# Optimization experiments

Measured on AMD Instinct MI355X. Metric: run time of the kernel, lower is better.

## Reference

```python
import jax, jax.numpy as jnp
import numpy as np

N = 100000
E = 1600000
D = 128
EPS = 1e-5


def setup_inputs() -> dict:
    key = jax.random.key(0)
    ks = jax.random.split(key, 6)
    X = jax.random.normal(ks[0], (N, D), dtype=jnp.float32)
    edge_weight = jax.random.uniform(ks[1], (E,), dtype=jnp.float32)
    W = jax.random.normal(ks[2], (2 * D, D), dtype=jnp.float32) * (1.0 / np.sqrt(2 * D))
    b = jax.random.normal(ks[3], (D,), dtype=jnp.float32) * 0.01
    gamma = jnp.ones((D,), dtype=jnp.float32)
    beta = jnp.zeros((D,), dtype=jnp.float32)
    edge_src = jax.random.randint(ks[4], (E,), 0, N, dtype=jnp.int32)
    edge_dst = jax.random.randint(ks[5], (E,), 0, N, dtype=jnp.int32)
    return {"X": X, "edge_weight": edge_weight, "W": W, "b": b,
            "gamma": gamma, "beta": beta,
            "edge_src": edge_src, "edge_dst": edge_dst}


def reference(X, edge_weight, W, b, gamma, beta, edge_src, edge_dst):
    # Pre-LayerNorm over feature dim
    mu = jnp.mean(X, axis=-1, keepdims=True)
    var = jnp.mean(jnp.square(X - mu), axis=-1, keepdims=True)
    H = (X - mu) * jax.lax.rsqrt(var + EPS) * gamma + beta
    # dropout is identity in eval mode
    # sparse neighbor aggregation: neigh[i] = sum_{e: dst[e]=i} w[e] * H[src[e]]
    msgs = edge_weight[:, None] * H[edge_src]          # [E, D]
    neigh = jax.ops.segment_sum(msgs, edge_dst, num_segments=X.shape[0])  # [N, D]
    cat = jnp.concatenate([H, neigh], axis=1)          # [N, 2D]
    out = cat @ W + b                                  # [N, D]
    out = jax.nn.relu(out)
    return out + X                                     # residual (in_dim == out_dim)
```

## Files before the change

### kernel.cpp

```cpp
#include <hip/hip_runtime.h>
#include <hip/hip_bf16.h>

#define N_NODES 100000
#define D 128
#define E_EDGES 1600000

#define BSHIFT 6
#define BROWS 64
#define NBUCK 1563
#define CAP 1536
#define NBLK_S 256
#define SBLK 1024
#define EPB (E_EDGES / NBLK_S)
#define LN_BLOCKS ((N_NODES + 15) / 16)

typedef __attribute__((ext_vector_type(8))) short bf16x8;
typedef __attribute__((ext_vector_type(8))) unsigned short ushort8;
typedef __attribute__((ext_vector_type(4))) float f32x4;

__device__ __forceinline__ float bf2f(unsigned short u) {
    unsigned int x = ((unsigned int)u) << 16;
    return __builtin_bit_cast(float, x);
}
__device__ __forceinline__ unsigned short f2bf(float f) {
    unsigned int x = __builtin_bit_cast(unsigned int, f);
    unsigned int lsb = (x >> 16) & 1u;
    x += 0x7fffu + lsb;
    return (unsigned short)(x >> 16);
}

__global__ __launch_bounds__(256) void wt_kernel(
    const float* __restrict__ W, unsigned short* __restrict__ Wt)
{
    int i = blockIdx.x * 1024 + threadIdx.x * 4;
    #pragma unroll
    for (int j = 0; j < 4; ++j) {
        int idx = i + j;
        int k = idx >> 7, col = idx & 127;
        Wt[col * 256 + k] = f2bf(W[idx]);
    }
}

__global__ __launch_bounds__(1024) void fused_ln_scatter(
    const float* __restrict__ X,
    const float* __restrict__ gamma,
    const float* __restrict__ beta,
    unsigned short* __restrict__ H,
    const int* __restrict__ esrc, const int* __restrict__ edst,
    const float* __restrict__ ew,
    unsigned int* __restrict__ gcur,
    uint2* __restrict__ bins)
{
    __shared__ unsigned int h[NBUCK];

    if (blockIdx.x < NBLK_S) {
        const int t = threadIdx.x;
        for (int i = t; i < NBUCK; i += SBLK) h[i] = 0;
        __syncthreads();

        const int base = blockIdx.x * EPB;
        for (int k = t; k < EPB; k += SBLK)
            atomicAdd(&h[edst[base + k] >> BSHIFT], 1u);
        __syncthreads();

        for (int i = t; i < NBUCK; i += SBLK) {
            unsigned int c = h[i];
            h[i] = c ? atomicAdd(&gcur[i], c) : 0u;
        }
        __syncthreads();

        for (int k = t; k < EPB; k += SBLK) {
            int e = base + k;
            int d = edst[e];
            int bkt = d >> BSHIFT;
            unsigned int p = atomicAdd(&h[bkt], 1u);
            if (p < CAP)
                bins[(size_t)bkt * CAP + p] =
                    make_uint2((unsigned int)esrc[e] |
                               ((unsigned int)(d & (BROWS - 1)) << 17),
                               __builtin_bit_cast(unsigned int, ew[e]));
        }
    } else {
        int wid  = (blockIdx.x - NBLK_S) * (SBLK / 64) + (threadIdx.x >> 6);
        int lane = threadIdx.x & 63;
        if (wid >= N_NODES) return;

        const float2 x2 = *reinterpret_cast<const float2*>(X + (size_t)wid * D + 2 * lane);
        float x0 = x2.x, x1 = x2.y;
        float s  = x0 + x1;
        float sq = x0 * x0 + x1 * x1;
        #pragma unroll
        for (int m = 1; m < 64; m <<= 1) {
            s  += __shfl_xor(s,  m);
            sq += __shfl_xor(sq, m);
        }
        float mu   = s * (1.0f / 128.0f);
        float var  = sq * (1.0f / 128.0f) - mu * mu;
        float rstd = rsqrtf(var + 1e-5f);

        const float2 g2 = *reinterpret_cast<const float2*>(gamma + 2 * lane);
        const float2 b2 = *reinterpret_cast<const float2*>(beta  + 2 * lane);

        ushort2 h2;
        h2.x = f2bf((x0 - mu) * rstd * g2.x + b2.x);
        h2.y = f2bf((x1 - mu) * rstd * g2.y + b2.y);
        *reinterpret_cast<ushort2*>(H + (size_t)wid * D + 2 * lane) = h2;
    }
}

__global__ __launch_bounds__(256) void sort_aggregate(
    const unsigned short* __restrict__ H,
    const uint2* __restrict__ bins,
    const unsigned int* __restrict__ gcur,
    unsigned short* __restrict__ nb)
{
    __shared__ uint2 srt[CAP];
    __shared__ unsigned int cnt[BROWS];
    __shared__ unsigned int cur[BROWS];
    __shared__ unsigned int starts[BROWS + 1];

    const int b = blockIdx.x;
    const int t = threadIdx.x;
    const unsigned int gbase = (unsigned int)b * CAP;
    const int nE = (int)min(gcur[b], (unsigned int)CAP);

    if (t < BROWS) cnt[t] = 0;
    __syncthreads();

    for (int k = t; k < nE; k += 256)
        atomicAdd(&cnt[bins[gbase + k].x >> 17], 1u);
    __syncthreads();

    if (t < BROWS) {
        unsigned int v = cnt[t], inc = v;
        #pragma unroll
        for (int off = 1; off < BROWS; off <<= 1) {
            unsigned int u = __shfl_up(inc, off);
            if (t >= off) inc += u;
        }
        unsigned int start = inc - v;
        starts[t] = start;
        cur[t] = start;
        if (t == BROWS - 1) starts[BROWS] = inc;
    }
    __syncthreads();

    for (int k = t; k < nE; k += 256) {
        uint2 r = bins[gbase + k];
        unsigned int p = atomicAdd(&cur[r.x >> 17], 1u);
        srt[p] = make_uint2(r.x & 0x1FFFFu, r.y);
    }
    __syncthreads();

    const int wv      = t >> 6;
    const int lane    = t & 63;
    const int quarter = lane >> 4;
    const int l15     = lane & 15;

    for (int j = 0; j < 16; ++j) {
        const int nl   = wv * 16 + j;
        const int node = b * BROWS + nl;
        if (node >= N_NODES) break;
        const int s = (int)starts[nl];
        const int n = (int)starts[nl + 1] - s;

        float a0 = 0.f, a1 = 0.f, a2 = 0.f, a3 = 0.f;
        float a4 = 0.f, a5 = 0.f, a6 = 0.f, a7 = 0.f;

        int k = 0;
        for (; k + 8 <= n; k += 8) {
            uint2 r0 = srt[s + k + quarter];
            uint2 r1 = srt[s + k + 4 + quarter];
            ushort8 h0 = *reinterpret_cast<const ushort8*>(H + (size_t)r0.x * D + 8 * l15);
            ushort8 h1 = *reinterpret_cast<const ushort8*>(H + (size_t)r1.x * D + 8 * l15);
            float w0 = __builtin_bit_cast(float, r0.y);
            float w1 = __builtin_bit_cast(float, r1.y);
            a0 += w0 * bf2f(h0[0]) + w1 * bf2f(h1[0]);
            a1 += w0 * bf2f(h0[1]) + w1 * bf2f(h1[1]);
            a2 += w0 * bf2f(h0[2]) + w1 * bf2f(h1[2]);
            a3 += w0 * bf2f(h0[3]) + w1 * bf2f(h1[3]);
            a4 += w0 * bf2f(h0[4]) + w1 * bf2f(h1[4]);
            a5 += w0 * bf2f(h0[5]) + w1 * bf2f(h1[5]);
            a6 += w0 * bf2f(h0[6]) + w1 * bf2f(h1[6]);
            a7 += w0 * bf2f(h0[7]) + w1 * bf2f(h1[7]);
        }
        if (k + 4 <= n) {
            uint2 r0 = srt[s + k + quarter];
            ushort8 h0 = *reinterpret_cast<const ushort8*>(H + (size_t)r0.x * D + 8 * l15);
            float w0 = __builtin_bit_cast(float, r0.y);
            a0 += w0 * bf2f(h0[0]); a1 += w0 * bf2f(h0[1]);
            a2 += w0 * bf2f(h0[2]); a3 += w0 * bf2f(h0[3]);
            a4 += w0 * bf2f(h0[4]); a5 += w0 * bf2f(h0[5]);
            a6 += w0 * bf2f(h0[6]); a7 += w0 * bf2f(h0[7]);
            k += 4;
        }
        if (k < n) {
            bool valid = (k + quarter) < n;
            uint2 r0 = srt[valid ? (s + k + quarter) : s];
            ushort8 h0 = *reinterpret_cast<const ushort8*>(H + (size_t)r0.x * D + 8 * l15);
            float w0 = valid ? __builtin_bit_cast(float, r0.y) : 0.f;
            a0 += w0 * bf2f(h0[0]); a1 += w0 * bf2f(h0[1]);
            a2 += w0 * bf2f(h0[2]); a3 += w0 * bf2f(h0[3]);
            a4 += w0 * bf2f(h0[4]); a5 += w0 * bf2f(h0[5]);
            a6 += w0 * bf2f(h0[6]); a7 += w0 * bf2f(h0[7]);
        }

        a0 += __shfl_xor(a0, 16); a0 += __shfl_xor(a0, 32);
        a1 += __shfl_xor(a1, 16); a1 += __shfl_xor(a1, 32);
        a2 += __shfl_xor(a2, 16); a2 += __shfl_xor(a2, 32);
        a3 += __shfl_xor(a3, 16); a3 += __shfl_xor(a3, 32);
        a4 += __shfl_xor(a4, 16); a4 += __shfl_xor(a4, 32);
        a5 += __shfl_xor(a5, 16); a5 += __shfl_xor(a5, 32);
        a6 += __shfl_xor(a6, 16); a6 += __shfl_xor(a6, 32);
        a7 += __shfl_xor(a7, 16); a7 += __shfl_xor(a7, 32);

        if (quarter == 0) {
            ushort8 ov;
            ov[0] = f2bf(a0); ov[1] = f2bf(a1); ov[2] = f2bf(a2); ov[3] = f2bf(a3);
            ov[4] = f2bf(a4); ov[5] = f2bf(a5); ov[6] = f2bf(a6); ov[7] = f2bf(a7);
            *reinterpret_cast<ushort8*>(nb + (size_t)node * D + 8 * l15) = ov;
        }
    }
}

#define ROWS_PER_BLOCK 128
#define STRIPS 8

__global__ __launch_bounds__(256) void gemm_kernel(
    const unsigned short* __restrict__ H,
    const unsigned short* __restrict__ nb,
    const unsigned short* __restrict__ Wt,
    const float* __restrict__ bias,
    const float* __restrict__ X,
    float* __restrict__ out)
{
    __shared__ unsigned short lds[16][256];

    const int tid  = threadIdx.x;
    const int w    = tid >> 6;
    const int lane = tid & 63;
    const int l15  = lane & 15;
    const int l4   = lane >> 4;

    bf16x8 bfrag[2][8];
    #pragma unroll
    for (int t = 0; t < 2; ++t) {
        const int col = 32 * w + 16 * t + l15;
        #pragma unroll
        for (int s = 0; s < 8; ++s)
            bfrag[t][s] = *reinterpret_cast<const bf16x8*>(
                Wt + (size_t)col * 256 + 32 * s + 8 * l4);
    }
    const float bias0 = bias[32 * w + l15];
    const float bias1 = bias[32 * w + 16 + l15];

    const int row0_blk = blockIdx.x * ROWS_PER_BLOCK;

    for (int strip = 0; strip < STRIPS; ++strip) {
        const int r0 = row0_blk + strip * 16;
        __syncthreads();

        {
            const int row  = tid >> 4;
            const int c8   = tid & 15;
            const int grow = r0 + row;
            char* ldsrow = (char*)&lds[row][0];
            const int key = (row & 7) << 4;

            uint4 hv = make_uint4(0u, 0u, 0u, 0u);
            uint4 nv = make_uint4(0u, 0u, 0u, 0u);
            if (grow < N_NODES) {
                hv = *reinterpret_cast<const uint4*>(H  + (size_t)grow * D + 8 * c8);
                nv = *reinterpret_cast<const uint4*>(nb + (size_t)grow * D + 8 * c8);
            }
            *reinterpret_cast<uint4*>(ldsrow + ((16 * c8) ^ key)) = hv;
            *reinterpret_cast<uint4*>(ldsrow + ((256 + 16 * c8) ^ key)) = nv;
        }
        __syncthreads();

        f32x4 acc0 = {0.f, 0.f, 0.f, 0.f};
        f32x4 acc1 = {0.f, 0.f, 0.f, 0.f};
        const char* ldsa = (const char*)&lds[l15][0];
        const int   akey = (l15 & 7) << 4;
        #pragma unroll
        for (int s = 0; s < 8; ++s) {
            bf16x8 afrag = *reinterpret_cast<const bf16x8*>(
                ldsa + ((64 * s + 16 * l4) ^ akey));
            acc0 = __builtin_amdgcn_mfma_f32_16x16x32_bf16(afrag, bfrag[0][s], acc0, 0, 0, 0);
            acc1 = __builtin_amdgcn_mfma_f32_16x16x32_bf16(afrag, bfrag[1][s], acc1, 0, 0, 0);
        }

        #pragma unroll
        for (int r = 0; r < 4; ++r) {
            const int grow = r0 + 4 * l4 + r;
            if (grow < N_NODES) {
                const size_t base = (size_t)grow * D;
                const int c0 = 32 * w + l15;
                float v0 = acc0[r] + bias0;
                v0 = v0 > 0.f ? v0 : 0.f;
                out[base + c0] = v0 + X[base + c0];
                const int c1 = c0 + 16;
                float v1 = acc1[r] + bias1;
                v1 = v1 > 0.f ? v1 : 0.f;
                out[base + c1] = v1 + X[base + c1];
            }
        }
    }
}

extern "C" void kernel_launch(void* const* d_in, const int* in_sizes, int n_in,
                              void* d_out, int out_size, void* d_ws, size_t ws_size,
                              hipStream_t stream)
{
    const float* X     = (const float*)d_in[0];
    const float* ew    = (const float*)d_in[1];
    const float* W     = (const float*)d_in[2];
    const float* b     = (const float*)d_in[3];
    const float* gamma = (const float*)d_in[4];
    const float* beta  = (const float*)d_in[5];
    const int* esrc = (const int*)d_in[6];
    const int* edst = (const int*)d_in[7];
    float* out = (float*)d_out;

    unsigned short* H  = (unsigned short*)d_ws;
    unsigned short* nb = H + (size_t)N_NODES * D;
    uint2* bins = (uint2*)(nb + (size_t)N_NODES * D);
    unsigned int* gcur = (unsigned int*)(bins + (size_t)NBUCK * CAP);
    unsigned short* Wt = (unsigned short*)(gcur + NBUCK + 1);

    hipMemsetAsync(gcur, 0, NBUCK * sizeof(unsigned int), stream);
    wt_kernel<<<32, 256, 0, stream>>>(W, Wt);
    fused_ln_scatter<<<NBLK_S + LN_BLOCKS, SBLK, 0, stream>>>(
        X, gamma, beta, H, esrc, edst, ew, gcur, bins);
    sort_aggregate<<<NBUCK, 256, 0, stream>>>(H, bins, gcur, nb);
    gemm_kernel<<<(N_NODES + ROWS_PER_BLOCK - 1) / ROWS_PER_BLOCK, 256, 0, stream>>>(
        H, nb, Wt, b, X, out);
}
```

Before: 147.3 us.

## Locally sort edges per block in LDS before coalesced bucket writes to global bins

The scatter blocks now stage their edge chunk in shared memory, build a block-local prefix sum over buckets, and write each bucket's run contiguously to global bins with padding to multiples of 8. Before, each edge was written to a scattered global slot. The aim is to replace those scattered 8-byte global writes with coalesced runs per bucket. Padding entries carry a zero weight and are skipped in sort_aggregate, which also means a real edge whose weight is exactly zero gets dropped (harmless for the sum). The costs are a larger global bin capacity, about 50KB of LDS per block, and extra prefix-scan work.

```diff
diff --git a/kernel.cpp b/kernel.cpp
--- a/kernel.cpp
+++ b/kernel.cpp
@@ -8,7 +8,9 @@
 #define BSHIFT 6
 #define BROWS 64
 #define NBUCK 1563
-#define CAP 1536
+#define NBUCKP 1600
+#define CAP 2304
+#define SRTCAP 1536
 #define NBLK_S 256
 #define SBLK 1024
 #define EPB (E_EDGES / NBLK_S)
@@ -51,21 +53,54 @@
     unsigned int* __restrict__ gcur,
     uint2* __restrict__ bins)
 {
-    __shared__ unsigned int h[NBUCK];
+    __shared__ uint2 ent[EPB];
+    __shared__ unsigned int hh[NBUCKP];
+    __shared__ unsigned int lofs[NBUCKP];
+    __shared__ unsigned int cur[NBUCKP];
+    __shared__ unsigned int ctot[32];
 
     if (blockIdx.x < NBLK_S) {
-        const int t = threadIdx.x;
-        for (int i = t; i < NBUCK; i += SBLK) h[i] = 0;
-        __syncthreads();
-
+        const int t    = threadIdx.x;
+        const int wv   = t >> 6;
+        const int lane = t & 63;
         const int base = blockIdx.x * EPB;
+
+        for (int i = t; i < NBUCKP; i += SBLK) hh[i] = 0;
+        __syncthreads();
         for (int k = t; k < EPB; k += SBLK)
-            atomicAdd(&h[edst[base + k] >> BSHIFT], 1u);
+            atomicAdd(&hh[edst[base + k] >> BSHIFT], 1u);
+        __syncthreads();
+
+        for (int c = wv; c < 25; c += 16) {
+            unsigned int v = hh[c * 64 + lane];
+            unsigned int inc = v;
+            #pragma unroll
+            for (int off = 1; off < 64; off <<= 1) {
+                unsigned int u = __shfl_up(inc, off);
+                if (lane >= off) inc += u;
+            }
+            lofs[c * 64 + lane] = inc - v;
+            if (lane == 63) ctot[c] = inc;
+        }
+        __syncthreads();
+        if (wv == 0) {
+            unsigned int v = (lane < 25) ? ctot[lane] : 0u;
+            unsigned int inc = v;
+            #pragma unroll
+            for (int off = 1; off < 32; off <<= 1) {
+                unsigned int u = __shfl_up(inc, off);
+                if (lane >= off) inc += u;
+            }
+            if (lane < 25) ctot[lane] = inc - v;
+        }
+        __syncthreads();
+        for (int i = t; i < NBUCKP; i += SBLK) lofs[i] += ctot[i >> 6];
         __syncthreads();
 
         for (int i = t; i < NBUCK; i += SBLK) {
-            unsigned int c = h[i];
-            h[i] = c ? atomicAdd(&gcur[i], c) : 0u;
+            unsigned int c = hh[i];
+            if (c) hh[i] = atomicAdd(&gcur[i], (c + 7u) & ~7u);
+            cur[i] = lofs[i];
         }
         __syncthreads();
 
@@ -73,12 +108,25 @@
             int e = base + k;
             int d = edst[e];
             int bkt = d >> BSHIFT;
-            unsigned int p = atomicAdd(&h[bkt], 1u);
-            if (p < CAP)
-                bins[(size_t)bkt * CAP + p] =
-                    make_uint2((unsigned int)esrc[e] |
-                               ((unsigned int)(d & (BROWS - 1)) << 17),
-                               __builtin_bit_cast(unsigned int, ew[e]));
+            unsigned int p = atomicAdd(&cur[bkt], 1u);
+            ent[p] = make_uint2((unsigned int)esrc[e] |
+                                ((unsigned int)(d & (BROWS - 1)) << 17),
+                                __builtin_bit_cast(unsigned int, ew[e]));
+        }
+        __syncthreads();
+
+        for (int b = wv; b < NBUCK; b += 16) {
+            unsigned int l0 = lofs[b];
+            unsigned int c  = cur[b] - l0;
+            if (!c) continue;
+            unsigned int cround = (c + 7u) & ~7u;
+            unsigned int gb = hh[b];
+            for (unsigned int j = lane; j < cround; j += 64) {
+                uint2 v = (j < c) ? ent[l0 + j] : make_uint2(0u, 0u);
+                unsigned int slot = gb + j;
+                if (slot < CAP)
+                    bins[(size_t)b * CAP + slot] = v;
+            }
         }
     } else {
         int wid  = (blockIdx.x - NBLK_S) * (SBLK / 64) + (threadIdx.x >> 6);
@@ -114,7 +162,7 @@
     const unsigned int* __restrict__ gcur,
     unsigned short* __restrict__ nb)
 {
-    __shared__ uint2 srt[CAP];
+    __shared__ uint2 srt[SRTCAP];
     __shared__ unsigned int cnt[BROWS];
     __shared__ unsigned int cur[BROWS];
     __shared__ unsigned int starts[BROWS + 1];
@@ -127,8 +175,10 @@
     if (t < BROWS) cnt[t] = 0;
     __syncthreads();
 
-    for (int k = t; k < nE; k += 256)
-        atomicAdd(&cnt[bins[gbase + k].x >> 17], 1u);
+    for (int k = t; k < nE; k += 256) {
+        uint2 r = bins[gbase + k];
+        if (r.y) atomicAdd(&cnt[r.x >> 17], 1u);
+    }
     __syncthreads();
 
     if (t < BROWS) {
@@ -147,8 +197,10 @@
 
     for (int k = t; k < nE; k += 256) {
         uint2 r = bins[gbase + k];
-        unsigned int p = atomicAdd(&cur[r.x >> 17], 1u);
-        srt[p] = make_uint2(r.x & 0x1FFFFu, r.y);
+        if (r.y) {
+            unsigned int p = atomicAdd(&cur[r.x >> 17], 1u);
+            if (p < SRTCAP) srt[p] = make_uint2(r.x & 0x1FFFFu, r.y);
+        }
     }
     __syncthreads();
 
```

After: 155.2 us. +5.4%, slower.

## Fuse neighbor aggregation with GEMM epilogue, keeping aggregates in LDS

Applied to the files above, without the earlier changes.

Merges the sort/aggregate kernel and the GEMM kernel into one kernel per 64-node bucket. The aggregated neighbor rows stay in swizzled shared memory and are fed straight into MFMA, while H rows are read directly from global memory. This removes the bf16 neighbor buffer write and re-read plus one kernel launch. In exchange it adds about 16KB of LDS and the Wt fragment registers to the aggregation kernel, which may reduce occupancy during the latency-bound gather phase.

```diff
diff --git a/kernel.cpp b/kernel.cpp
--- a/kernel.cpp
+++ b/kernel.cpp
@@ -108,13 +108,17 @@
     }
 }
 
-__global__ __launch_bounds__(256) void sort_aggregate(
+__global__ __launch_bounds__(256) void agg_gemm(
     const unsigned short* __restrict__ H,
     const uint2* __restrict__ bins,
     const unsigned int* __restrict__ gcur,
-    unsigned short* __restrict__ nb)
+    const unsigned short* __restrict__ Wt,
+    const float* __restrict__ bias,
+    const float* __restrict__ X,
+    float* __restrict__ out)
 {
     __shared__ uint2 srt[CAP];
+    __shared__ unsigned short nbt[BROWS][D];
     __shared__ unsigned int cnt[BROWS];
     __shared__ unsigned int cur[BROWS];
     __shared__ unsigned int starts[BROWS + 1];
@@ -124,6 +128,24 @@
     const unsigned int gbase = (unsigned int)b * CAP;
     const int nE = (int)min(gcur[b], (unsigned int)CAP);
 
+    const int w    = t >> 6;
+    const int lane = t & 63;
+    const int l15  = lane & 15;
+    const int l4   = lane >> 4;
+    const int quarter = lane >> 4;
+
+    bf16x8 bfrag[2][8];
+    #pragma unroll
+    for (int tt = 0; tt < 2; ++tt) {
+        const int col = 32 * w + 16 * tt + l15;
+        #pragma unroll
+        for (int s = 0; s < 8; ++s)
+            bfrag[tt][s] = *reinterpret_cast<const bf16x8*>(
+                Wt + (size_t)col * 256 + 32 * s + 8 * l4);
+    }
+    const float bias0 = bias[32 * w + l15];
+    const float bias1 = bias[32 * w + 16 + l15];
+
     if (t < BROWS) cnt[t] = 0;
     __syncthreads();
 
@@ -152,13 +174,8 @@
     }
     __syncthreads();
 
-    const int wv      = t >> 6;
-    const int lane    = t & 63;
-    const int quarter = lane >> 4;
-    const int l15     = lane & 15;
-
     for (int j = 0; j < 16; ++j) {
-        const int nl   = wv * 16 + j;
+        const int nl   = w * 16 + j;
         const int node = b * BROWS + nl;
         if (node >= N_NODES) break;
         const int s = (int)starts[nl];
@@ -218,91 +235,48 @@
             ushort8 ov;
             ov[0] = f2bf(a0); ov[1] = f2bf(a1); ov[2] = f2bf(a2); ov[3] = f2bf(a3);
             ov[4] = f2bf(a4); ov[5] = f2bf(a5); ov[6] = f2bf(a6); ov[7] = f2bf(a7);
-            *reinterpret_cast<ushort8*>(nb + (size_t)node * D + 8 * l15) = ov;
-        }
-    }
-}
-
-#define ROWS_PER_BLOCK 128
-#define STRIPS 8
-
-__global__ __launch_bounds__(256) void gemm_kernel(
-    const unsigned short* __restrict__ H,
-    const unsigned short* __restrict__ nb,
-    const unsigned short* __restrict__ Wt,
-    const float* __restrict__ bias,
-    const float* __restrict__ X,
-    float* __restrict__ out)
-{
-    __shared__ unsigned short lds[16][256];
-
-    const int tid  = threadIdx.x;
-    const int w    = tid >> 6;
-    const int lane = tid & 63;
-    const int l15  = lane & 15;
-    const int l4   = lane >> 4;
-
-    bf16x8 bfrag[2][8];
-    #pragma unroll
-    for (int t = 0; t < 2; ++t) {
-        const int col = 32 * w + 16 * t + l15;
-        #pragma unroll
-        for (int s = 0; s < 8; ++s)
-            bfrag[t][s] = *reinterpret_cast<const bf16x8*>(
-                Wt + (size_t)col * 256 + 32 * s + 8 * l4);
-    }
-    const float bias0 = bias[32 * w + l15];
-    const float bias1 = bias[32 * w + 16 + l15];
-
-    const int row0_blk = blockIdx.x * ROWS_PER_BLOCK;
-
-    for (int strip = 0; strip < STRIPS; ++strip) {
-        const int r0 = row0_blk + strip * 16;
-        __syncthreads();
-
-        {
-            const int row  = tid >> 4;
-            const int c8   = tid & 15;
-            const int grow = r0 + row;
-            char* ldsrow = (char*)&lds[row][0];
-            const int key = (row & 7) << 4;
-
-            uint4 hv = make_uint4(0u, 0u, 0u, 0u);
-            uint4 nv = make_uint4(0u, 0u, 0u, 0u);
-            if (grow < N_NODES) {
-                hv = *reinterpret_cast<const uint4*>(H  + (size_t)grow * D + 8 * c8);
-                nv = *reinterpret_cast<const uint4*>(nb + (size_t)grow * D + 8 * c8);
-            }
-            *reinterpret_cast<uint4*>(ldsrow + ((16 * c8) ^ key)) = hv;
-            *reinterpret_cast<uint4*>(ldsrow + ((256 + 16 * c8) ^ key)) = nv;
-        }
-        __syncthreads();
+            char* p = (char*)&nbt[nl][0];
+            *reinterpret_cast<ushort8*>(p + ((16 * l15) ^ ((nl & 7) << 4))) = ov;
+        }
+    }
+    __syncthreads();
+
+    for (int strip = 0; strip < 4; ++strip) {
+        const int r0s  = strip * 16;
+        const int arow = b * BROWS + r0s + l15;
+        const size_t hrow = (size_t)(arow < N_NODES ? arow : N_NODES - 1) * D;
 
         f32x4 acc0 = {0.f, 0.f, 0.f, 0.f};
         f32x4 acc1 = {0.f, 0.f, 0.f, 0.f};
-        const char* ldsa = (const char*)&lds[l15][0];
-        const int   akey = (l15 & 7) << 4;
-        #pragma unroll
-        for (int s = 0; s < 8; ++s) {
-            bf16x8 afrag = *reinterpret_cast<const bf16x8*>(
-                ldsa + ((64 * s + 16 * l4) ^ akey));
-            acc0 = __builtin_amdgcn_mfma_f32_16x16x32_bf16(afrag, bfrag[0][s], acc0, 0, 0, 0);
-            acc1 = __builtin_amdgcn_mfma_f32_16x16x32_bf16(afrag, bfrag[1][s], acc1, 0, 0, 0);
+
+        #pragma unroll
+        for (int s = 0; s < 4; ++s) {
+            bf16x8 af = *reinterpret_cast<const bf16x8*>(H + hrow + 32 * s + 8 * l4);
+            acc0 = __builtin_amdgcn_mfma_f32_16x16x32_bf16(af, bfrag[0][s], acc0, 0, 0, 0);
+            acc1 = __builtin_amdgcn_mfma_f32_16x16x32_bf16(af, bfrag[1][s], acc1, 0, 0, 0);
+        }
+        const char* np  = (const char*)&nbt[r0s + l15][0];
+        const int  nkey = ((r0s + l15) & 7) << 4;
+        #pragma unroll
+        for (int s = 0; s < 4; ++s) {
+            bf16x8 af = *reinterpret_cast<const bf16x8*>(np + ((64 * s + 16 * l4) ^ nkey));
+            acc0 = __builtin_amdgcn_mfma_f32_16x16x32_bf16(af, bfrag[0][4 + s], acc0, 0, 0, 0);
+            acc1 = __builtin_amdgcn_mfma_f32_16x16x32_bf16(af, bfrag[1][4 + s], acc1, 0, 0, 0);
         }
 
         #pragma unroll
         for (int r = 0; r < 4; ++r) {
-            const int grow = r0 + 4 * l4 + r;
-            if (grow < N_NODES) {
-                const size_t base = (size_t)grow * D;
+            const int gr = b * BROWS + r0s + 4 * l4 + r;
+            if (gr < N_NODES) {
+                const size_t basei = (size_t)gr * D;
                 const int c0 = 32 * w + l15;
                 float v0 = acc0[r] + bias0;
                 v0 = v0 > 0.f ? v0 : 0.f;
-                out[base + c0] = v0 + X[base + c0];
+                out[basei + c0] = v0 + X[basei + c0];
                 const int c1 = c0 + 16;
                 float v1 = acc1[r] + bias1;
                 v1 = v1 > 0.f ? v1 : 0.f;
-                out[base + c1] = v1 + X[base + c1];
+                out[basei + c1] = v1 + X[basei + c1];
             }
         }
     }
@@ -322,9 +296,8 @@
     const int* edst = (const int*)d_in[7];
     float* out = (float*)d_out;
 
-    unsigned short* H  = (unsigned short*)d_ws;
-    unsigned short* nb = H + (size_t)N_NODES * D;
-    uint2* bins = (uint2*)(nb + (size_t)N_NODES * D);
+    unsigned short* H = (unsigned short*)d_ws;
+    uint2* bins = (uint2*)(H + (size_t)N_NODES * D);
     unsigned int* gcur = (unsigned int*)(bins + (size_t)NBUCK * CAP);
     unsigned short* Wt = (unsigned short*)(gcur + NBUCK + 1);
 
@@ -332,7 +305,5 @@
     wt_kernel<<<32, 256, 0, stream>>>(W, Wt);
     fused_ln_scatter<<<NBLK_S + LN_BLOCKS, SBLK, 0, stream>>>(
         X, gamma, beta, H, esrc, edst, ew, gcur, bins);
-    sort_aggregate<<<NBUCK, 256, 0, stream>>>(H, bins, gcur, nb);
-    gemm_kernel<<<(N_NODES + ROWS_PER_BLOCK - 1) / ROWS_PER_BLOCK, 256, 0, stream>>>(
-        H, nb, Wt, b, X, out);
-}
+    agg_gemm<<<NBUCK, 256, 0, stream>>>(H, bins, gcur, Wt, b, X, out);
+}
```

Result: slower. 153.4 us (+4.1%).
